# Optimization experiments

Measured on AMD Instinct MI355X. Metric: run time of the kernel, lower is better.

Reference implementation:

```python
import jax, jax.numpy as jnp
import numpy as np

N_NODES = 10000
N_EDGES = 80000
LATENT = 128
OUT_SIZE = 3
NODE_F = 12
EDGE_F = 7
STEPS = 15
LN_EPS = 1e-5


def _mlp(x, W0, b0, W1, b1, W2, b2):
    h = jax.nn.relu(x @ W0 + b0)
    h = jax.nn.relu(h @ W1 + b1)
    return h @ W2 + b2


def _ln(x, g, b):
    m = jnp.mean(x, axis=-1, keepdims=True)
    v = jnp.mean(jnp.square(x - m), axis=-1, keepdims=True)
    return (x - m) * jax.lax.rsqrt(v + LN_EPS) * g + b


def _forward(node_features, edge_features, senders, receivers,
             enW0, enb0, enW1, enb1, enW2, enb2, eng, enbe,
             eeW0, eeb0, eeW1, eeb1, eeW2, eeb2, eeg, eebe,
             beW0, beb0, beW1, beb1, beW2, beb2, beg, bebe,
             bnW0, bnb0, bnW1, bnb1, bnW2, bnb2, bng, bnbe,
             dW0, db0, dW1, db1, dW2, db2):
    # Encoder: node and mesh-edge MLPs with LayerNorm
    nl = _ln(_mlp(node_features, enW0, enb0, enW1, enb1, enW2, enb2), eng, enbe)  # [N, L]
    el = _ln(_mlp(edge_features, eeW0, eeb0, eeW1, eeb1, eeW2, eeb2), eeg, eebe)  # [E, L]

    # Processor: 15 GraphNetBlocks with residual connections, scanned over stacked params
    def block(carry, p):
        n, e = carry
        (eW0, eb0, eW1, eb1, eW2, eb2, eg, ebe,
         nW0, nb0, nW1, nb1, nW2, nb2, ng, nbe) = p
        feat = jnp.concatenate([n[senders], n[receivers], e], axis=-1)  # [E, 3L]
        new_e = _ln(_mlp(feat, eW0, eb0, eW1, eb1, eW2, eb2), eg, ebe)  # [E, L]
        agg = jax.ops.segment_sum(new_e, receivers, num_segments=N_NODES)  # [N, L]
        new_n = _ln(_mlp(jnp.concatenate([n, agg], axis=-1), nW0, nb0, nW1, nb1, nW2, nb2), ng, nbe)
        return (n + new_n, e + new_e), None

    xs = (beW0, beb0, beW1, beb1, beW2, beb2, beg, bebe,
          bnW0, bnb0, bnW1, bnb1, bnW2, bnb2, bng, bnbe)
    (nl, el), _ = jax.lax.scan(jax.checkpoint(block), (nl, el), xs)

    # Decoder: MLP without LayerNorm
    return _mlp(nl, dW0, db0, dW1, db1, dW2, db2)  # [N, OUT_SIZE]


def setup_inputs() -> dict:
    ks = iter(jax.random.split(jax.random.key(0), 32))

    def W(*shape):
        return jax.random.normal(next(ks), shape, jnp.float32) * (1.0 / np.sqrt(shape[-2]))

    z = lambda *s: jnp.zeros(s, jnp.float32)
    o = lambda *s: jnp.ones(s, jnp.float32)
    d = {}
    d['node_features'] = jax.random.normal(next(ks), (N_NODES, NODE_F), jnp.float32)
    d['edge_features'] = jax.random.normal(next(ks), (N_EDGES, EDGE_F), jnp.float32)
    d['senders'] = jax.random.randint(next(ks), (N_EDGES,), 0, N_NODES, jnp.int32)
    d['receivers'] = jax.random.randint(next(ks), (N_EDGES,), 0, N_NODES, jnp.int32)
    d.update(enW0=W(NODE_F, LATENT), enb0=z(LATENT), enW1=W(LATENT, LATENT), enb1=z(LATENT),
             enW2=W(LATENT, LATENT), enb2=z(LATENT), eng=o(LATENT), enbe=z(LATENT))
    d.update(eeW0=W(EDGE_F, LATENT), eeb0=z(LATENT), eeW1=W(LATENT, LATENT), eeb1=z(LATENT),
             eeW2=W(LATENT, LATENT), eeb2=z(LATENT), eeg=o(LATENT), eebe=z(LATENT))
    d.update(beW0=W(STEPS, 3 * LATENT, LATENT), beb0=z(STEPS, LATENT),
             beW1=W(STEPS, LATENT, LATENT), beb1=z(STEPS, LATENT),
             beW2=W(STEPS, LATENT, LATENT), beb2=z(STEPS, LATENT),
             beg=o(STEPS, LATENT), bebe=z(STEPS, LATENT))
    d.update(bnW0=W(STEPS, 2 * LATENT, LATENT), bnb0=z(STEPS, LATENT),
             bnW1=W(STEPS, LATENT, LATENT), bnb1=z(STEPS, LATENT),
             bnW2=W(STEPS, LATENT, LATENT), bnb2=z(STEPS, LATENT),
             bng=o(STEPS, LATENT), bnbe=z(STEPS, LATENT))
    d.update(dW0=W(LATENT, LATENT), db0=z(LATENT), dW1=W(LATENT, LATENT), db1=z(LATENT),
             dW2=W(LATENT, OUT_SIZE), db2=z(OUT_SIZE))
    return d


def reference(node_features, edge_features, senders, receivers,
              enW0, enb0, enW1, enb1, enW2, enb2, eng, enbe,
              eeW0, eeb0, eeW1, eeb1, eeW2, eeb2, eeg, eebe,
              beW0, beb0, beW1, beb1, beW2, beb2, beg, bebe,
              bnW0, bnb0, bnW1, bnb1, bnW2, bnb2, bng, bnbe,
              dW0, db0, dW1, db1, dW2, db2):
    return _forward(node_features, edge_features, senders, receivers,
                    enW0, enb0, enW1, enb1, enW2, enb2, eng, enbe,
                    eeW0, eeb0, eeW1, eeb1, eeW2, eeb2, eeg, eebe,
                    beW0, beb0, beW1, beb1, beW2, beb2, beg, bebe,
                    bnW0, bnb0, bnW1, bnb1, bnW2, bnb2, bng, bnbe,
                    dW0, db0, dW1, db1, dW2, db2)
```

## Files before the change

kernel.cpp:

```cpp
#include <hip/hip_runtime.h>
#include <hip/hip_bf16.h>
#include <stdint.h>

#define N_NODES 10000
#define N_EDGES 80000
#define L 128
#define STEPS 15
#define LN_EPS 1e-5f
#define NTHR 256
#define H_STRIDE 272

typedef short short8 __attribute__((ext_vector_type(8)));
typedef float floatx4 __attribute__((ext_vector_type(4)));

__device__ __forceinline__ float bf2f(const __hip_bfloat16 x) {
    return __bfloat162float(x);
}
__device__ __forceinline__ float ldmix(const void* p, int idx, int isf32) {
    return isf32 ? ((const float*)p)[idx]
                 : bf2f(((const __hip_bfloat16*)p)[idx]);
}

__global__ void detect_dtype(const uint32_t* __restrict__ nf, int* cnt) {
    int c = 0;
    for (int i = blockIdx.x * blockDim.x + threadIdx.x; i < 60000;
         i += gridDim.x * blockDim.x) {
        const uint32_t w = nf[i];
        c += (((w >> 7) & 0xFF) >= 0xC6) + (((w >> 23) & 0xFF) >= 0xC6);
    }
    atomicAdd(cnt, c);
}

#define N_TMATS 14
struct TAll {
    const void* src[N_TMATS];
    long long cum[N_TMATS + 1];
    int K[N_TMATS], N[N_TMATS], Kpad[N_TMATS];
};

__global__ void transpose_all(TAll a, const int* __restrict__ cnt,
                              __hip_bfloat16* __restrict__ pool) {
    const int isf32 = (*cnt > 1000);
    const long long total = a.cum[N_TMATS];
    for (long long i = blockIdx.x * (long long)blockDim.x + threadIdx.x;
         i < total; i += gridDim.x * (long long)blockDim.x) {
        int e = 0;
        #pragma unroll 1
        for (int j = 1; j < N_TMATS; j++) if (i >= a.cum[j]) e = j;
        const long long r = i - a.cum[e];
        const int per = a.N[e] * a.Kpad[e];
        const int m = (int)(r / per);
        const int r2 = (int)(r - (long long)m * per);
        const int nn = r2 / a.Kpad[e];
        const int kk = r2 - nn * a.Kpad[e];
        float v = 0.f;
        if (kk < a.K[e]) v = ldmix(a.src[e], (m * a.K[e] + kk) * a.N[e] + nn, isf32);
        pool[i] = __float2bfloat16(v);
    }
}

__global__ void convert_feats(const void* __restrict__ nf,
                              const void* __restrict__ ef,
                              const int* __restrict__ cnt,
                              const int* __restrict__ elist,
                              __hip_bfloat16* __restrict__ fN,
                              __hip_bfloat16* __restrict__ fE)
{
    const int isf32 = (*cnt > 1000);
    const int totN = N_NODES * 32;
    const int totE = N_EDGES * 32;
    for (int i = blockIdx.x * blockDim.x + threadIdx.x; i < totN + totE;
         i += gridDim.x * blockDim.x) {
        if (i < totN) {
            const int r = i >> 5, c = i & 31;
            fN[i] = __float2bfloat16(c < 12 ? ldmix(nf, r * 12 + c, isf32) : 0.f);
        } else {
            const int j = i - totN;
            const int r = j >> 5, c = j & 31;
            const int e = elist[r];
            fE[j] = __float2bfloat16(c < 7 ? ldmix(ef, e * 7 + c, isf32) : 0.f);
        }
    }
}

__global__ void csr_hist(const int* __restrict__ rcv, int* __restrict__ deg) {
    for (int i = blockIdx.x * blockDim.x + threadIdx.x; i < N_EDGES;
         i += gridDim.x * blockDim.x)
        atomicAdd(&deg[rcv[i]], 1);
}

__global__ void csr_scan(const int* __restrict__ deg, int* __restrict__ rowptr,
                         int* __restrict__ cursor) {
    __shared__ int part[256];
    __shared__ int partx[257];
    const int t = threadIdx.x;
    int s = 0;
    for (int j = 0; j < 40; j++) {
        const int i = t * 40 + j;
        if (i < N_NODES) s += deg[i];
    }
    part[t] = s;
    __syncthreads();
    if (t == 0) {
        int r = 0;
        for (int k = 0; k < 256; k++) { partx[k] = r; r += part[k]; }
        partx[256] = r;
    }
    __syncthreads();
    int run = partx[t];
    for (int j = 0; j < 40; j++) {
        const int i = t * 40 + j;
        if (i < N_NODES) {
            rowptr[i] = run;
            cursor[i] = run;
            run += deg[i];
        }
    }
    if (t == 255) rowptr[N_NODES] = partx[256];
}

__global__ void csr_scatter(const int* __restrict__ rcv, int* __restrict__ cursor,
                            int* __restrict__ elist) {
    for (int i = blockIdx.x * blockDim.x + threadIdx.x; i < N_EDGES;
         i += gridDim.x * blockDim.x) {
        const int p = atomicAdd(&cursor[rcv[i]], 1);
        elist[p] = i;
    }
}

__global__ void sort_meta(const int* __restrict__ snd, const int* __restrict__ rcv,
                          const int* __restrict__ elist,
                          int* __restrict__ ssnd, int* __restrict__ srcv) {
    for (int i = blockIdx.x * blockDim.x + threadIdx.x; i < N_EDGES;
         i += gridDim.x * blockDim.x) {
        const int e = elist[i];
        ssnd[i] = snd[e];
        srcv[i] = rcv[e];
    }
}

__global__ __launch_bounds__(256)
void csr_agg(const int* __restrict__ rowptr,
             const __hip_bfloat16* __restrict__ ln16,
             __hip_bfloat16* __restrict__ agg16)
{
    const int g = threadIdx.x >> 5;
    const int lane = threadIdx.x & 31;
    const int v = blockIdx.x * 8 + g;
    if (v >= N_NODES) return;
    const int c0 = lane * 4;
    float s0 = 0.f, s1 = 0.f, s2 = 0.f, s3 = 0.f;
    int j = rowptr[v];
    const int en = rowptr[v + 1];
    for (; j + 1 < en; j += 2) {
        union { uint2 w; __hip_bfloat16 h[4]; } u0, u1;
        u0.w = *(const uint2*)(ln16 + (size_t)j * L + c0);
        u1.w = *(const uint2*)(ln16 + (size_t)(j + 1) * L + c0);
        s0 += bf2f(u0.h[0]); s1 += bf2f(u0.h[1]); s2 += bf2f(u0.h[2]); s3 += bf2f(u0.h[3]);
        s0 += bf2f(u1.h[0]); s1 += bf2f(u1.h[1]); s2 += bf2f(u1.h[2]); s3 += bf2f(u1.h[3]);
    }
    for (; j < en; j++) {
        union { uint2 w; __hip_bfloat16 h[4]; } u;
        u.w = *(const uint2*)(ln16 + (size_t)j * L + c0);
        s0 += bf2f(u.h[0]); s1 += bf2f(u.h[1]); s2 += bf2f(u.h[2]); s3 += bf2f(u.h[3]);
    }
    union { uint2 w; __hip_bfloat16 h[4]; } o;
    o.h[0] = __float2bfloat16(s0); o.h[1] = __float2bfloat16(s1);
    o.h[2] = __float2bfloat16(s2); o.h[3] = __float2bfloat16(s3);
    *(uint2*)(agg16 + (size_t)v * L + c0) = o.w;
}

enum AMode { A_PLAIN = 0, A_FEAT = 1, A_CAT = 2 };
enum Epi   { E_LN_STORE = 0, E_LN_EDGE = 1, E_LN_NODE = 2, E_DEC = 3 };

template <int AMODE, int EPI, int NL, int RT, int MINW>
__global__ __launch_bounds__(NTHR, MINW)
void fused_mlp(const __hip_bfloat16* __restrict__ A, int lda, int M, int K0,
               const __hip_bfloat16* __restrict__ WT0,
               const __hip_bfloat16* __restrict__ WT1,
               const __hip_bfloat16* __restrict__ WT2,
               const void* __restrict__ b0,
               const void* __restrict__ b1,
               const void* __restrict__ b2,
               const void* __restrict__ g,
               const void* __restrict__ beta,
               int poff,
               const int* __restrict__ cnt,
               const __hip_bfloat16* __restrict__ n16,
               const __hip_bfloat16* __restrict__ e16s,
               const __hip_bfloat16* __restrict__ agg16,
               const int* __restrict__ ssnd,
               const int* __restrict__ srcv,
               float* res32,
               __hip_bfloat16* res16,
               __hip_bfloat16* __restrict__ lnout,
               const void* __restrict__ dW,
               const void* __restrict__ db,
               void* __restrict__ dout)
{
    constexpr int BMv   = 64 * RT;
    constexpr int HW    = RT * 16 * H_STRIDE;
    constexpr int WSOFF = 4 * HW;
    __shared__ __align__(16) char lds[WSOFF + 10240];
    char* AsB = lds;
    char* WsB = lds + WSOFF;

    const int tid  = threadIdx.x;
    const int wv   = tid >> 6;
    const int lane = tid & 63;
    const int quad = lane >> 4;
    const int m15  = lane & 15;
    const int row0 = blockIdx.x * BMv;
    const int isf32 = (*cnt > 1000);

    char* hw = lds + wv * HW;

    const int boff = m15 * 80 + quad * 16;
    int aoff[RT];
    #pragma unroll
    for (int rt = 0; rt < RT; rt++)
        aoff[rt] = (wv * 16 * RT + rt * 16 + m15) * 80 + quad * 16;

    const int aq = tid & 3;
    int arow[RT], sidx[RT], ridx[RT];
    #pragma unroll
    for (int i2 = 0; i2 < RT; i2++) {
        arow[i2] = (i2 * NTHR + tid) >> 2;
        if constexpr (AMODE == A_FEAT) {
            const int rg = row0 + arow[i2];
            sidx[i2] = (rg < M) ? ssnd[rg] : 0;
            ridx[i2] = (rg < M) ? srcv[rg] : 0;
        }
    }

    auto loadA = [&](int k0, int i2) -> int4 {
        const int rg = row0 + arow[i2];
        int4 av = make_int4(0, 0, 0, 0);
        if (rg < M) {
            if constexpr (AMODE == A_PLAIN) {
                av = *(const int4*)(A + (size_t)rg * lda + k0 + aq * 8);
            } else if constexpr (AMODE == A_FEAT) {
                const __hip_bfloat16* sp;
                if (k0 < 2 * L) {
                    const int nd = (k0 < L) ? sidx[i2] : ridx[i2];
                    sp = n16 + (size_t)nd * L + (k0 & (L - 1)) + aq * 8;
                } else {
                    sp = e16s + (size_t)rg * L + (k0 - 2 * L) + aq * 8;
                }
                av = *(const int4*)sp;
            } else {
                const __hip_bfloat16* sp = (k0 < L)
                    ? n16   + (size_t)rg * L + k0 + aq * 8
                    : agg16 + (size_t)rg * L + (k0 - L) + aq * 8;
                av = *(const int4*)sp;
            }
        }
        return av;
    };
    auto loadW = [&](const __hip_bfloat16* WT, int ksz, int k0, int i2) -> int4 {
        const int flat = i2 * NTHR + tid;
        return *(const int4*)(WT + (size_t)(flat >> 2) * ksz + k0 + (flat & 3) * 8);
    };

    floatx4 acc[RT][8];

    #pragma unroll
    for (int rt = 0; rt < RT; rt++)
        #pragma unroll
        for (int ct = 0; ct < 8; ct++) acc[rt][ct] = (floatx4)0.f;

    int4 pA[RT], pW[2];
    #pragma unroll
    for (int i2 = 0; i2 < RT; i2++) pA[i2] = loadA(0, i2);
    pW[0] = loadW(WT0, K0, 0, 0);
    pW[1] = loadW(WT0, K0, 0, 1);

    for (int k0 = 0; k0 < K0; k0 += 32) {
        #pragma unroll
        for (int i2 = 0; i2 < RT; i2++)
            *(int4*)(AsB + arow[i2] * 80 + aq * 16) = pA[i2];
        #pragma unroll
        for (int i2 = 0; i2 < 2; i2++) {
            const int flat = i2 * NTHR + tid;
            *(int4*)(WsB + (flat >> 2) * 80 + (flat & 3) * 16) = pW[i2];
        }
        __syncthreads();
        if (k0 + 32 < K0) {
            #pragma unroll
            for (int i2 = 0; i2 < RT; i2++) pA[i2] = loadA(k0 + 32, i2);
            pW[0] = loadW(WT0, K0, k0 + 32, 0);
            pW[1] = loadW(WT0, K0, k0 + 32, 1);
        }
        short8 a[RT];
        #pragma unroll
        for (int rt = 0; rt < RT; rt++) a[rt] = *(const short8*)(AsB + aoff[rt]);
        #pragma unroll
        for (int ct = 0; ct < 8; ct++) {
            const short8 b = *(const short8*)(WsB + boff + ct * 1280);
            #pragma unroll
            for (int rt = 0; rt < RT; rt++)
                acc[rt][ct] = __builtin_amdgcn_mfma_f32_16x16x32_bf16(a[rt], b, acc[rt][ct], 0, 0, 0);
        }
        __syncthreads();
    }
    {
        float bb[8];
        #pragma unroll
        for (int ct = 0; ct < 8; ct++) bb[ct] = ldmix(b0, poff + ct * 16 + m15, isf32);
        #pragma unroll
        for (int rt = 0; rt < RT; rt++)
            #pragma unroll
            for (int ct = 0; ct < 8; ct++)
                #pragma unroll
                for (int i = 0; i < 4; i++) {
                    const int rl = rt * 16 + quad * 4 + i;
                    const int col = ct * 16 + m15;
                    *(__hip_bfloat16*)(hw + rl * H_STRIDE + col * 2) =
                        __float2bfloat16(fmaxf(acc[rt][ct][i] + bb[ct], 0.f));
                }
    }

    {
        #pragma unroll
        for (int rt = 0; rt < RT; rt++)
            #pragma unroll
            for (int ct = 0; ct < 8; ct++) acc[rt][ct] = (floatx4)0.f;
        short8 af[RT][4];
        #pragma unroll
        for (int rt = 0; rt < RT; rt++)
            #pragma unroll
            for (int c = 0; c < 4; c++)
                af[rt][c] = *(const short8*)(hw + (rt * 16 + m15) * H_STRIDE + c * 64 + quad * 16);
        int4 qW[2];
        qW[0] = loadW(WT1, L, 0, 0);
        qW[1] = loadW(WT1, L, 0, 1);
        for (int c = 0; c < 4; c++) {
            #pragma unroll
            for (int i2 = 0; i2 < 2; i2++) {
                const int flat = i2 * NTHR + tid;
                *(int4*)(WsB + (flat >> 2) * 80 + (flat & 3) * 16) = qW[i2];
            }
            __syncthreads();
            if (c < 3) {
                qW[0] = loadW(WT1, L, (c + 1) * 32, 0);
                qW[1] = loadW(WT1, L, (c + 1) * 32, 1);
            }
            #pragma unroll
            for (int ct = 0; ct < 8; ct++) {
                const short8 b = *(const short8*)(WsB + boff + ct * 1280);
                #pragma unroll
                for (int rt = 0; rt < RT; rt++)
                    acc[rt][ct] = __builtin_amdgcn_mfma_f32_16x16x32_bf16(af[rt][c], b, acc[rt][ct], 0, 0, 0);
            }
            __syncthreads();
        }
        float bb[8];
        #pragma unroll
        for (int ct = 0; ct < 8; ct++) bb[ct] = ldmix(b1, poff + ct * 16 + m15, isf32);
        #pragma unroll
        for (int rt = 0; rt < RT; rt++)
            #pragma unroll
            for (int ct = 0; ct < 8; ct++)
                #pragma unroll
                for (int i = 0; i < 4; i++) {
                    const int rl = rt * 16 + quad * 4 + i;
                    const int col = ct * 16 + m15;
                    *(__hip_bfloat16*)(hw + rl * H_STRIDE + col * 2) =
                        __float2bfloat16(fmaxf(acc[rt][ct][i] + bb[ct], 0.f));
                }
    }

    if constexpr (NL == 3) {
        #pragma unroll
        for (int rt = 0; rt < RT; rt++)
            #pragma unroll
            for (int ct = 0; ct < 8; ct++) acc[rt][ct] = (floatx4)0.f;
        short8 af[RT][4];
        #pragma unroll
        for (int rt = 0; rt < RT; rt++)
            #pragma unroll
            for (int c = 0; c < 4; c++)
                af[rt][c] = *(const short8*)(hw + (rt * 16 + m15) * H_STRIDE + c * 64 + quad * 16);
        int4 qW[2];
        qW[0] = loadW(WT2, L, 0, 0);
        qW[1] = loadW(WT2, L, 0, 1);
        for (int c = 0; c < 4; c++) {
            #pragma unroll
            for (int i2 = 0; i2 < 2; i2++) {
                const int flat = i2 * NTHR + tid;
                *(int4*)(WsB + (flat >> 2) * 80 + (flat & 3) * 16) = qW[i2];
            }
            __syncthreads();
            if (c < 3) {
                qW[0] = loadW(WT2, L, (c + 1) * 32, 0);
                qW[1] = loadW(WT2, L, (c + 1) * 32, 1);
            }
            #pragma unroll
            for (int ct = 0; ct < 8; ct++) {
                const short8 b = *(const short8*)(WsB + boff + ct * 1280);
                #pragma unroll
                for (int rt = 0; rt < RT; rt++)
                    acc[rt][ct] = __builtin_amdgcn_mfma_f32_16x16x32_bf16(af[rt][c], b, acc[rt][ct], 0, 0, 0);
            }
            __syncthreads();
        }
        float bb[8], gg[8], be[8];
        #pragma unroll
        for (int ct = 0; ct < 8; ct++) {
            bb[ct] = ldmix(b2,   poff + ct * 16 + m15, isf32);
            gg[ct] = ldmix(g,    poff + ct * 16 + m15, isf32);
            be[ct] = ldmix(beta, poff + ct * 16 + m15, isf32);
        }
        #pragma unroll
        for (int rt = 0; rt < RT; rt++) {
            #pragma unroll
            for (int i = 0; i < 4; i++) {
                float t[8], s = 0.f, s2 = 0.f;
                #pragma unroll
                for (int ct = 0; ct < 8; ct++) {
                    t[ct] = acc[rt][ct][i] + bb[ct];
                    s  += t[ct];
                    s2 += t[ct] * t[ct];
                }
                #pragma unroll
                for (int m = 1; m < 16; m <<= 1) {
                    s  += __shfl_xor(s,  m, 64);
                    s2 += __shfl_xor(s2, m, 64);
                }
                const float mean = s * (1.f / 128.f);
                const float var  = s2 * (1.f / 128.f) - mean * mean;
                const float inv  = rsqrtf(fmaxf(var, 0.f) + LN_EPS);
                const int rl = wv * 16 * RT + rt * 16 + quad * 4 + i;
                const int rg = row0 + rl;
                if (rg < M) {
                    #pragma unroll
                    for (int ct = 0; ct < 8; ct++) {
                        const int col = ct * 16 + m15;
                        const float o = (t[ct] - mean) * inv * gg[ct] + be[ct];
                        const size_t idx = (size_t)rg * L + col;
                        if constexpr (EPI == E_LN_STORE) {
                            res32[idx] = o;
                            if (res16) res16[idx] = __float2bfloat16(o);
                        } else if constexpr (EPI == E_LN_NODE) {
                            const float nw = res32[idx] + o;
                            res32[idx] = nw;
                            res16[idx] = __float2bfloat16(nw);
                        } else {
                            const float nw = res32[idx] + o;
                            res32[idx] = nw;
                            res16[idx] = __float2bfloat16(nw);
                            lnout[idx] = __float2bfloat16(o);
                        }
                    }
                }
            }
        }
    } else {
        __syncthreads();
        float* Wl = (float*)WsB;
        for (int i = tid; i < 3 * L; i += NTHR) {
            const int o = i / L, k = i - o * L;
            Wl[o * L + k] = ldmix(dW, k * 3 + o, isf32);
        }
        __syncthreads();
        if (tid < BMv) {
            const int rg = row0 + tid;
            if (rg < M) {
                const int wave = tid / (16 * RT);
                const int rw   = tid - wave * 16 * RT;
                const __hip_bfloat16* hr =
                    (const __hip_bfloat16*)(lds + wave * HW + rw * H_STRIDE);
                float s0 = ldmix(db, 0, isf32);
                float s1 = ldmix(db, 1, isf32);
                float s2 = ldmix(db, 2, isf32);
                #pragma unroll 8
                for (int k = 0; k < L; k++) {
                    const float hv = bf2f(hr[k]);
                    s0 += hv * Wl[k];
                    s1 += hv * Wl[L + k];
                    s2 += hv * Wl[2 * L + k];
                }
                if (isf32) {
                    float* o = (float*)dout;
                    o[rg * 3 + 0] = s0; o[rg * 3 + 1] = s1; o[rg * 3 + 2] = s2;
                } else {
                    __hip_bfloat16* o = (__hip_bfloat16*)dout;
                    o[rg * 3 + 0] = __float2bfloat16(s0);
                    o[rg * 3 + 1] = __float2bfloat16(s1);
                    o[rg * 3 + 2] = __float2bfloat16(s2);
                }
            }
        }
    }
}

extern "C" void kernel_launch(void* const* d_in, const int* in_sizes, int n_in,
                              void* d_out, int out_size, void* d_ws, size_t ws_size,
                              hipStream_t stream)
{
    (void)in_sizes; (void)n_in; (void)out_size; (void)ws_size;
    const int* snd = (const int*)d_in[2];
    const int* rcv = (const int*)d_in[3];

    char* ws = (char*)d_ws;
    int* cnt = (int*)ws;                              ws += 256;
    auto takeB = [&](size_t el) {
        __hip_bfloat16* p = (__hip_bfloat16*)ws;
        ws += ((el * 2 + 255) & ~255ull);
        return p;
    };
    auto takeF = [&](size_t el) {
        float* p = (float*)ws;
        ws += ((el * 4 + 255) & ~255ull);
        return p;
    };
    auto takeI = [&](size_t el) {
        int* p = (int*)ws;
        ws += ((el * 4 + 255) & ~255ull);
        return p;
    };

    const int srcIdx[N_TMATS] = {4, 6, 8, 12, 14, 16, 20, 22, 24, 28, 30, 32, 36, 38};
    const int tK[N_TMATS]    = {12, 128, 128, 7, 128, 128, 384, 128, 128, 256, 128, 128, 128, 128};
    const int tKp[N_TMATS]   = {32, 128, 128, 32, 128, 128, 384, 128, 128, 256, 128, 128, 128, 128};
    const int tNm[N_TMATS]   = {1, 1, 1, 1, 1, 1, STEPS, STEPS, STEPS, STEPS, STEPS, STEPS, 1, 1};
    TAll ta;
    long long cum = 0;
    __hip_bfloat16* wmat[N_TMATS];
    __hip_bfloat16* wpool = (__hip_bfloat16*)ws;
    for (int j = 0; j < N_TMATS; j++) {
        ta.src[j] = d_in[srcIdx[j]];
        ta.cum[j] = cum;
        ta.K[j] = tK[j]; ta.N[j] = 128; ta.Kpad[j] = tKp[j];
        wmat[j] = wpool + cum;
        cum += (long long)tNm[j] * 128 * tKp[j];
    }
    ta.cum[N_TMATS] = cum;
    ws += ((cum * 2 + 255) & ~255ull);

    float* n32 = takeF((size_t)N_NODES * L);
    float* e32 = takeF((size_t)N_EDGES * L);
    __hip_bfloat16* n16   = takeB((size_t)N_NODES * L);
    __hip_bfloat16* e16   = takeB((size_t)N_EDGES * L);
    __hip_bfloat16* ln16  = takeB((size_t)N_EDGES * L);
    __hip_bfloat16* agg16 = takeB((size_t)N_NODES * L);
    __hip_bfloat16* fN16  = takeB((size_t)N_NODES * 32);
    __hip_bfloat16* fE16  = takeB((size_t)N_EDGES * 32);
    int* deg    = takeI(N_NODES);
    int* rowptr = takeI(N_NODES + 1);
    int* cursor = takeI(N_NODES);
    int* elist  = takeI(N_EDGES);
    int* ssnd   = takeI(N_EDGES);
    int* srcv   = takeI(N_EDGES);

    const dim3 blk(NTHR);
    const dim3 grdE((N_EDGES + 63) / 64);
    const dim3 grdN((N_NODES + 63) / 64);

    (void)hipMemsetAsync(cnt, 0, sizeof(int), stream);
    (void)hipMemsetAsync(deg, 0, N_NODES * sizeof(int), stream);
    detect_dtype<<<dim3(64), blk, 0, stream>>>((const uint32_t*)d_in[0], cnt);
    transpose_all<<<dim3(512), blk, 0, stream>>>(ta, cnt, wpool);

    csr_hist<<<dim3(80), blk, 0, stream>>>(rcv, deg);
    csr_scan<<<dim3(1), blk, 0, stream>>>(deg, rowptr, cursor);
    csr_scatter<<<dim3(80), blk, 0, stream>>>(rcv, cursor, elist);
    sort_meta<<<dim3(80), blk, 0, stream>>>(snd, rcv, elist, ssnd, srcv);
    convert_feats<<<dim3(256), blk, 0, stream>>>(d_in[0], d_in[1], cnt, elist, fN16, fE16);

    fused_mlp<A_PLAIN, E_LN_STORE, 3, 1, 3><<<grdE, blk, 0, stream>>>(
        fE16, 32, N_EDGES, 32, wmat[3], wmat[4], wmat[5],
        d_in[13], d_in[15], d_in[17], d_in[18], d_in[19], 0, cnt,
        nullptr, nullptr, nullptr, nullptr, nullptr,
        e32, e16, nullptr, nullptr, nullptr, nullptr);
    fused_mlp<A_PLAIN, E_LN_STORE, 3, 1, 3><<<grdN, blk, 0, stream>>>(
        fN16, 32, N_NODES, 32, wmat[0], wmat[1], wmat[2],
        d_in[5], d_in[7], d_in[9], d_in[10], d_in[11], 0, cnt,
        nullptr, nullptr, nullptr, nullptr, nullptr,
        n32, n16, nullptr, nullptr, nullptr, nullptr);

    for (int s = 0; s < STEPS; s++) {
        const int po = s * L;
        fused_mlp<A_FEAT, E_LN_EDGE, 3, 1, 3><<<grdE, blk, 0, stream>>>(
            nullptr, 0, N_EDGES, 384,
            wmat[6] + (size_t)s * 128 * 384,
            wmat[7] + (size_t)s * 128 * 128,
            wmat[8] + (size_t)s * 128 * 128,
            d_in[21], d_in[23], d_in[25], d_in[26], d_in[27], po, cnt,
            n16, e16, nullptr, ssnd, srcv,
            e32, e16, ln16, nullptr, nullptr, nullptr);
        csr_agg<<<dim3((N_NODES + 7) / 8), blk, 0, stream>>>(rowptr, ln16, agg16);
        fused_mlp<A_CAT, E_LN_NODE, 3, 1, 3><<<grdN, blk, 0, stream>>>(
            nullptr, 0, N_NODES, 256,
            wmat[9]  + (size_t)s * 128 * 256,
            wmat[10] + (size_t)s * 128 * 128,
            wmat[11] + (size_t)s * 128 * 128,
            d_in[29], d_in[31], d_in[33], d_in[34], d_in[35], po, cnt,
            n16, nullptr, agg16, nullptr, nullptr,
            n32, n16, nullptr, nullptr, nullptr, nullptr);
    }

    fused_mlp<A_PLAIN, E_DEC, 2, 1, 3><<<grdN, blk, 0, stream>>>(
        n16, L, N_NODES, L, wmat[12], wmat[13], nullptr,
        d_in[37], d_in[39], nullptr, nullptr, nullptr, 0, cnt,
        nullptr, nullptr, nullptr, nullptr, nullptr,
        nullptr, nullptr, nullptr, d_in[40], d_in[41], d_out);
}
```

Before: 1.328 ms.

## Pre-swizzle weights into MFMA fragment order and double-buffer LDS weight tiles

The weight transpose kernel now writes weights in the exact per-lane MFMA B-fragment order, so LDS stores and reads are contiguous 16-byte per-lane accesses. The MLP kernel loads A fragments directly from global memory into registers instead of staging them through LDS. It double-buffers 64-wide K sections of weights in LDS, which roughly halves the barrier count and overlaps the next section's load with the current MFMAs. K0 becomes a template parameter and the RT row-tiling option is removed, at the cost of more LDS per block and scattered direct global gathers for the A operand.

```diff
diff --git a/kernel.cpp b/kernel.cpp
--- a/kernel.cpp
+++ b/kernel.cpp
@@ -50,11 +50,16 @@
         const long long r = i - a.cum[e];
         const int per = a.N[e] * a.Kpad[e];
         const int m = (int)(r / per);
-        const int r2 = (int)(r - (long long)m * per);
-        const int nn = r2 / a.Kpad[e];
-        const int kk = r2 - nn * a.Kpad[e];
+        int r2 = (int)(r - (long long)m * per);
+        const int c2   = r2 >> 12;
+        const int rem  = r2 & 4095;
+        const int ct   = rem >> 9;
+        const int lane = (rem >> 3) & 63;
+        const int j    = rem & 7;
+        const int k    = c2 * 32 + (lane >> 4) * 8 + j;
+        const int col  = ct * 16 + (lane & 15);
         float v = 0.f;
-        if (kk < a.K[e]) v = ldmix(a.src[e], (m * a.K[e] + kk) * a.N[e] + nn, isf32);
+        if (k < a.K[e]) v = ldmix(a.src[e], (m * a.K[e] + k) * a.N[e] + col, isf32);
         pool[i] = __float2bfloat16(v);
     }
 }
@@ -173,9 +178,9 @@
 enum AMode { A_PLAIN = 0, A_FEAT = 1, A_CAT = 2 };
 enum Epi   { E_LN_STORE = 0, E_LN_EDGE = 1, E_LN_NODE = 2, E_DEC = 3 };
 
-template <int AMODE, int EPI, int NL, int RT, int MINW>
-__global__ __launch_bounds__(NTHR, MINW)
-void fused_mlp(const __hip_bfloat16* __restrict__ A, int lda, int M, int K0,
+template <int AMODE, int EPI, int NL, int K0>
+__global__ __launch_bounds__(NTHR, 3)
+void fused_mlp(const __hip_bfloat16* __restrict__ A, int lda, int M,
                const __hip_bfloat16* __restrict__ WT0,
                const __hip_bfloat16* __restrict__ WT1,
                const __hip_bfloat16* __restrict__ WT2,
@@ -198,211 +203,160 @@
                const void* __restrict__ db,
                void* __restrict__ dout)
 {
-    constexpr int BMv   = 64 * RT;
-    constexpr int HW    = RT * 16 * H_STRIDE;
-    constexpr int WSOFF = 4 * HW;
-    __shared__ __align__(16) char lds[WSOFF + 10240];
-    char* AsB = lds;
-    char* WsB = lds + WSOFF;
+    __shared__ __align__(16) char lds[17408 + 32768];
+    char* wbuf = lds + 17408;
 
     const int tid  = threadIdx.x;
     const int wv   = tid >> 6;
     const int lane = tid & 63;
     const int quad = lane >> 4;
     const int m15  = lane & 15;
-    const int row0 = blockIdx.x * BMv;
+    const int row0 = blockIdx.x * 64;
     const int isf32 = (*cnt > 1000);
 
-    char* hw = lds + wv * HW;
-
-    const int boff = m15 * 80 + quad * 16;
-    int aoff[RT];
+    char* hw = lds + wv * 4352;
+
+    const int rw = row0 + wv * 16 + m15;
+    const int rc = rw < M ? rw : M - 1;
+
+    int sI = 0, rI = 0;
+    if constexpr (AMODE == A_FEAT) { sI = ssnd[rc]; rI = srcv[rc]; }
+
+    auto aFrag = [&](int kchunk) -> short8 {
+        const int k0 = kchunk * 32 + quad * 8;
+        const __hip_bfloat16* sp;
+        if constexpr (AMODE == A_PLAIN) {
+            sp = A + (size_t)rc * lda + k0;
+        } else if constexpr (AMODE == A_FEAT) {
+            if (k0 < L)          sp = n16  + (size_t)sI * L + k0;
+            else if (k0 < 2 * L) sp = n16  + (size_t)rI * L + (k0 - L);
+            else                 sp = e16s + (size_t)rc * L + (k0 - 2 * L);
+        } else {
+            if (k0 < L) sp = n16   + (size_t)rc * L + k0;
+            else        sp = agg16 + (size_t)rc * L + (k0 - L);
+        }
+        return *(const short8*)sp;
+    };
+    auto loadW = [&](const __hip_bfloat16* secPtr, int ch, int4* wr) {
+        #pragma unroll
+        for (int it = 0; it < 4; it++)
+            if (it < 2 * ch)
+                wr[it] = *(const int4*)(secPtr + (size_t)wv * ch * 1024 + it * 512 + lane * 8);
+    };
+    auto storeW = [&](int buf, int ch, const int4* wr) {
+        #pragma unroll
+        for (int it = 0; it < 4; it++)
+            if (it < 2 * ch)
+                *(int4*)(wbuf + buf * 16384 + wv * ch * 2048 + it * 1024 + lane * 16) = wr[it];
+    };
+    auto bread = [&](int buf, int kc, int ct) -> short8 {
+        return *(const short8*)(wbuf + buf * 16384 + kc * 8192 + ct * 1024 + lane * 16);
+    };
+
+    constexpr int CH0 = (K0 == 32) ? 1 : 2;
+    constexpr int S0  = (K0 == 32) ? 1 : (K0 / 64);
+
+    int4 wreg[4];
+    short8 aF[2];
+    int buf = 0;
+    floatx4 acc[8];
+
     #pragma unroll
-    for (int rt = 0; rt < RT; rt++)
-        aoff[rt] = (wv * 16 * RT + rt * 16 + m15) * 80 + quad * 16;
-
-    const int aq = tid & 3;
-    int arow[RT], sidx[RT], ridx[RT];
-    #pragma unroll
-    for (int i2 = 0; i2 < RT; i2++) {
-        arow[i2] = (i2 * NTHR + tid) >> 2;
-        if constexpr (AMODE == A_FEAT) {
-            const int rg = row0 + arow[i2];
-            sidx[i2] = (rg < M) ? ssnd[rg] : 0;
-            ridx[i2] = (rg < M) ? srcv[rg] : 0;
-        }
-    }
-
-    auto loadA = [&](int k0, int i2) -> int4 {
-        const int rg = row0 + arow[i2];
-        int4 av = make_int4(0, 0, 0, 0);
-        if (rg < M) {
-            if constexpr (AMODE == A_PLAIN) {
-                av = *(const int4*)(A + (size_t)rg * lda + k0 + aq * 8);
-            } else if constexpr (AMODE == A_FEAT) {
-                const __hip_bfloat16* sp;
-                if (k0 < 2 * L) {
-                    const int nd = (k0 < L) ? sidx[i2] : ridx[i2];
-                    sp = n16 + (size_t)nd * L + (k0 & (L - 1)) + aq * 8;
-                } else {
-                    sp = e16s + (size_t)rg * L + (k0 - 2 * L) + aq * 8;
-                }
-                av = *(const int4*)sp;
-            } else {
-                const __hip_bfloat16* sp = (k0 < L)
-                    ? n16   + (size_t)rg * L + k0 + aq * 8
-                    : agg16 + (size_t)rg * L + (k0 - L) + aq * 8;
-                av = *(const int4*)sp;
-            }
-        }
-        return av;
-    };
-    auto loadW = [&](const __hip_bfloat16* WT, int ksz, int k0, int i2) -> int4 {
-        const int flat = i2 * NTHR + tid;
-        return *(const int4*)(WT + (size_t)(flat >> 2) * ksz + k0 + (flat & 3) * 8);
-    };
-
-    floatx4 acc[RT][8];
-
-    #pragma unroll
-    for (int rt = 0; rt < RT; rt++)
-        #pragma unroll
-        for (int ct = 0; ct < 8; ct++) acc[rt][ct] = (floatx4)0.f;
-
-    int4 pA[RT], pW[2];
-    #pragma unroll
-    for (int i2 = 0; i2 < RT; i2++) pA[i2] = loadA(0, i2);
-    pW[0] = loadW(WT0, K0, 0, 0);
-    pW[1] = loadW(WT0, K0, 0, 1);
-
-    for (int k0 = 0; k0 < K0; k0 += 32) {
-        #pragma unroll
-        for (int i2 = 0; i2 < RT; i2++)
-            *(int4*)(AsB + arow[i2] * 80 + aq * 16) = pA[i2];
-        #pragma unroll
-        for (int i2 = 0; i2 < 2; i2++) {
-            const int flat = i2 * NTHR + tid;
-            *(int4*)(WsB + (flat >> 2) * 80 + (flat & 3) * 16) = pW[i2];
-        }
+    for (int ct = 0; ct < 8; ct++) acc[ct] = (floatx4)0.f;
+
+    loadW(WT0, CH0, wreg);
+    aF[0] = aFrag(0);
+    if constexpr (CH0 == 2) aF[1] = aFrag(1);
+
+    for (int sec = 0; sec < S0; sec++) {
+        storeW(buf, CH0, wreg);
         __syncthreads();
-        if (k0 + 32 < K0) {
-            #pragma unroll
-            for (int i2 = 0; i2 < RT; i2++) pA[i2] = loadA(k0 + 32, i2);
-            pW[0] = loadW(WT0, K0, k0 + 32, 0);
-            pW[1] = loadW(WT0, K0, k0 + 32, 1);
-        }
-        short8 a[RT];
-        #pragma unroll
-        for (int rt = 0; rt < RT; rt++) a[rt] = *(const short8*)(AsB + aoff[rt]);
-        #pragma unroll
-        for (int ct = 0; ct < 8; ct++) {
-            const short8 b = *(const short8*)(WsB + boff + ct * 1280);
-            #pragma unroll
-            for (int rt = 0; rt < RT; rt++)
-                acc[rt][ct] = __builtin_amdgcn_mfma_f32_16x16x32_bf16(a[rt], b, acc[rt][ct], 0, 0, 0);
-        }
-        __syncthreads();
+        const short8 a0 = aF[0];
+        const short8 a1 = aF[1];
+        if (sec + 1 < S0) {
+            loadW(WT0 + (size_t)(sec + 1) * CH0 * 4096, CH0, wreg);
+            aF[0] = aFrag((sec + 1) * CH0);
+            if constexpr (CH0 == 2) aF[1] = aFrag((sec + 1) * CH0 + 1);
+        } else {
+            loadW(WT1, 2, wreg);
+        }
+        #pragma unroll
+        for (int ct = 0; ct < 8; ct++)
+            acc[ct] = __builtin_amdgcn_mfma_f32_16x16x32_bf16(a0, bread(buf, 0, ct), acc[ct], 0, 0, 0);
+        if constexpr (CH0 == 2) {
+            #pragma unroll
+            for (int ct = 0; ct < 8; ct++)
+                acc[ct] = __builtin_amdgcn_mfma_f32_16x16x32_bf16(a1, bread(buf, 1, ct), acc[ct], 0, 0, 0);
+        }
+        buf ^= 1;
     }
     {
         float bb[8];
         #pragma unroll
         for (int ct = 0; ct < 8; ct++) bb[ct] = ldmix(b0, poff + ct * 16 + m15, isf32);
         #pragma unroll
-        for (int rt = 0; rt < RT; rt++)
-            #pragma unroll
-            for (int ct = 0; ct < 8; ct++)
+        for (int ct = 0; ct < 8; ct++)
+            #pragma unroll
+            for (int i = 0; i < 4; i++) {
+                const int rl = quad * 4 + i;
+                const int col = ct * 16 + m15;
+                *(__hip_bfloat16*)(hw + rl * H_STRIDE + col * 2) =
+                    __float2bfloat16(fmaxf(acc[ct][i] + bb[ct], 0.f));
+            }
+    }
+
+    {
+        #pragma unroll
+        for (int ct = 0; ct < 8; ct++) acc[ct] = (floatx4)0.f;
+        short8 af[4];
+        #pragma unroll
+        for (int c = 0; c < 4; c++)
+            af[c] = *(const short8*)(hw + m15 * H_STRIDE + c * 64 + quad * 16);
+        for (int sec = 0; sec < 2; sec++) {
+            storeW(buf, 2, wreg);
+            __syncthreads();
+            if (sec == 0)            loadW(WT1 + 8192, 2, wreg);
+            else if constexpr (NL == 3) loadW(WT2, 2, wreg);
+            #pragma unroll
+            for (int kc = 0; kc < 2; kc++)
                 #pragma unroll
-                for (int i = 0; i < 4; i++) {
-                    const int rl = rt * 16 + quad * 4 + i;
-                    const int col = ct * 16 + m15;
-                    *(__hip_bfloat16*)(hw + rl * H_STRIDE + col * 2) =
-                        __float2bfloat16(fmaxf(acc[rt][ct][i] + bb[ct], 0.f));
-                }
-    }
-
-    {
-        #pragma unroll
-        for (int rt = 0; rt < RT; rt++)
-            #pragma unroll
-            for (int ct = 0; ct < 8; ct++) acc[rt][ct] = (floatx4)0.f;
-        short8 af[RT][4];
-        #pragma unroll
-        for (int rt = 0; rt < RT; rt++)
-            #pragma unroll
-            for (int c = 0; c < 4; c++)
-                af[rt][c] = *(const short8*)(hw + (rt * 16 + m15) * H_STRIDE + c * 64 + quad * 16);
-        int4 qW[2];
-        qW[0] = loadW(WT1, L, 0, 0);
-        qW[1] = loadW(WT1, L, 0, 1);
-        for (int c = 0; c < 4; c++) {
-            #pragma unroll
-            for (int i2 = 0; i2 < 2; i2++) {
-                const int flat = i2 * NTHR + tid;
-                *(int4*)(WsB + (flat >> 2) * 80 + (flat & 3) * 16) = qW[i2];
+                for (int ct = 0; ct < 8; ct++)
+                    acc[ct] = __builtin_amdgcn_mfma_f32_16x16x32_bf16(
+                        af[sec * 2 + kc], bread(buf, kc, ct), acc[ct], 0, 0, 0);
+            buf ^= 1;
+        }
+        float bb[8];
+        #pragma unroll
+        for (int ct = 0; ct < 8; ct++) bb[ct] = ldmix(b1, poff + ct * 16 + m15, isf32);
+        #pragma unroll
+        for (int ct = 0; ct < 8; ct++)
+            #pragma unroll
+            for (int i = 0; i < 4; i++) {
+                const int rl = quad * 4 + i;
+                const int col = ct * 16 + m15;
+                *(__hip_bfloat16*)(hw + rl * H_STRIDE + col * 2) =
+                    __float2bfloat16(fmaxf(acc[ct][i] + bb[ct], 0.f));
             }
+    }
+
+    if constexpr (NL == 3) {
+        #pragma unroll
+        for (int ct = 0; ct < 8; ct++) acc[ct] = (floatx4)0.f;
+        short8 af[4];
+        #pragma unroll
+        for (int c = 0; c < 4; c++)
+            af[c] = *(const short8*)(hw + m15 * H_STRIDE + c * 64 + quad * 16);
+        for (int sec = 0; sec < 2; sec++) {
+            storeW(buf, 2, wreg);
             __syncthreads();
-            if (c < 3) {
-                qW[0] = loadW(WT1, L, (c + 1) * 32, 0);
-                qW[1] = loadW(WT1, L, (c + 1) * 32, 1);
-            }
-            #pragma unroll
-            for (int ct = 0; ct < 8; ct++) {
-                const short8 b = *(const short8*)(WsB + boff + ct * 1280);
+            if (sec == 0) loadW(WT2 + 8192, 2, wreg);
+            #pragma unroll
+            for (int kc = 0; kc < 2; kc++)
                 #pragma unroll
-                for (int rt = 0; rt < RT; rt++)
-                    acc[rt][ct] = __builtin_amdgcn_mfma_f32_16x16x32_bf16(af[rt][c], b, acc[rt][ct], 0, 0, 0);
-            }
-            __syncthreads();
-        }
-        float bb[8];
-        #pragma unroll
-        for (int ct = 0; ct < 8; ct++) bb[ct] = ldmix(b1, poff + ct * 16 + m15, isf32);
-        #pragma unroll
-        for (int rt = 0; rt < RT; rt++)
-            #pragma unroll
-            for (int ct = 0; ct < 8; ct++)
-                #pragma unroll
-                for (int i = 0; i < 4; i++) {
-                    const int rl = rt * 16 + quad * 4 + i;
-                    const int col = ct * 16 + m15;
-                    *(__hip_bfloat16*)(hw + rl * H_STRIDE + col * 2) =
-                        __float2bfloat16(fmaxf(acc[rt][ct][i] + bb[ct], 0.f));
-                }
-    }
-
-    if constexpr (NL == 3) {
-        #pragma unroll
-        for (int rt = 0; rt < RT; rt++)
-            #pragma unroll
-            for (int ct = 0; ct < 8; ct++) acc[rt][ct] = (floatx4)0.f;
-        short8 af[RT][4];
-        #pragma unroll
-        for (int rt = 0; rt < RT; rt++)
-            #pragma unroll
-            for (int c = 0; c < 4; c++)
-                af[rt][c] = *(const short8*)(hw + (rt * 16 + m15) * H_STRIDE + c * 64 + quad * 16);
-        int4 qW[2];
-        qW[0] = loadW(WT2, L, 0, 0);
-        qW[1] = loadW(WT2, L, 0, 1);
-        for (int c = 0; c < 4; c++) {
-            #pragma unroll
-            for (int i2 = 0; i2 < 2; i2++) {
-                const int flat = i2 * NTHR + tid;
-                *(int4*)(WsB + (flat >> 2) * 80 + (flat & 3) * 16) = qW[i2];
-            }
-            __syncthreads();
-            if (c < 3) {
-                qW[0] = loadW(WT2, L, (c + 1) * 32, 0);
-                qW[1] = loadW(WT2, L, (c + 1) * 32, 1);
-            }
-            #pragma unroll
-            for (int ct = 0; ct < 8; ct++) {
-                const short8 b = *(const short8*)(WsB + boff + ct * 1280);
-                #pragma unroll
-                for (int rt = 0; rt < RT; rt++)
-                    acc[rt][ct] = __builtin_amdgcn_mfma_f32_16x16x32_bf16(af[rt][c], b, acc[rt][ct], 0, 0, 0);
-            }
-            __syncthreads();
+                for (int ct = 0; ct < 8; ct++)
+                    acc[ct] = __builtin_amdgcn_mfma_f32_16x16x32_bf16(
+                        af[sec * 2 + kc], bread(buf, kc, ct), acc[ct], 0, 0, 0);
+            buf ^= 1;
         }
         float bb[8], gg[8], be[8];
         #pragma unroll
@@ -412,64 +366,58 @@
             be[ct] = ldmix(beta, poff + ct * 16 + m15, isf32);
         }
         #pragma unroll
-        for (int rt = 0; rt < RT; rt++) {
-            #pragma unroll
-            for (int i = 0; i < 4; i++) {
-                float t[8], s = 0.f, s2 = 0.f;
+        for (int i = 0; i < 4; i++) {
+            float t[8], s = 0.f, s2 = 0.f;
+            #pragma unroll
+            for (int ct = 0; ct < 8; ct++) {
+                t[ct] = acc[ct][i] + bb[ct];
+                s  += t[ct];
+                s2 += t[ct] * t[ct];
+            }
+            #pragma unroll
+            for (int m = 1; m < 16; m <<= 1) {
+                s  += __shfl_xor(s,  m, 64);
+                s2 += __shfl_xor(s2, m, 64);
+            }
+            const float mean = s * (1.f / 128.f);
+            const float var  = s2 * (1.f / 128.f) - mean * mean;
+            const float inv  = rsqrtf(fmaxf(var, 0.f) + LN_EPS);
+            const int rg = row0 + wv * 16 + quad * 4 + i;
+            if (rg < M) {
                 #pragma unroll
                 for (int ct = 0; ct < 8; ct++) {
-                    t[ct] = acc[rt][ct][i] + bb[ct];
-                    s  += t[ct];
-                    s2 += t[ct] * t[ct];
-                }
-                #pragma unroll
-                for (int m = 1; m < 16; m <<= 1) {
-                    s  += __shfl_xor(s,  m, 64);
-                    s2 += __shfl_xor(s2, m, 64);
-                }
-                const float mean = s * (1.f / 128.f);
-                const float var  = s2 * (1.f / 128.f) - mean * mean;
-                const float inv  = rsqrtf(fmaxf(var, 0.f) + LN_EPS);
-                const int rl = wv * 16 * RT + rt * 16 + quad * 4 + i;
-                const int rg = row0 + rl;
-                if (rg < M) {
-                    #pragma unroll
-                    for (int ct = 0; ct < 8; ct++) {
-                        const int col = ct * 16 + m15;
-                        const float o = (t[ct] - mean) * inv * gg[ct] + be[ct];
-                        const size_t idx = (size_t)rg * L + col;
-                        if constexpr (EPI == E_LN_STORE) {
-                            res32[idx] = o;
-                            if (res16) res16[idx] = __float2bfloat16(o);
-                        } else if constexpr (EPI == E_LN_NODE) {
-                            const float nw = res32[idx] + o;
-                            res32[idx] = nw;
-                            res16[idx] = __float2bfloat16(nw);
-                        } else {
-                            const float nw = res32[idx] + o;
-                            res32[idx] = nw;
-                            res16[idx] = __float2bfloat16(nw);
-                            lnout[idx] = __float2bfloat16(o);
-                        }
+                    const int col = ct * 16 + m15;
+                    const float o = (t[ct] - mean) * inv * gg[ct] + be[ct];
+                    const size_t idx = (size_t)rg * L + col;
+                    if constexpr (EPI == E_LN_STORE) {
+                        res32[idx] = o;
+                        if (res16) res16[idx] = __float2bfloat16(o);
+                    } else if constexpr (EPI == E_LN_NODE) {
+                        const float nw = res32[idx] + o;
+                        res32[idx] = nw;
+                        res16[idx] = __float2bfloat16(nw);
+                    } else {
+                        const float nw = res32[idx] + o;
+                        res32[idx] = nw;
+                        res16[idx] = __float2bfloat16(nw);
+                        lnout[idx] = __float2bfloat16(o);
                     }
                 }
             }
         }
     } else {
         __syncthreads();
-        float* Wl = (float*)WsB;
+        float* Wl = (float*)wbuf;
         for (int i = tid; i < 3 * L; i += NTHR) {
             const int o = i / L, k = i - o * L;
             Wl[o * L + k] = ldmix(dW, k * 3 + o, isf32);
         }
         __syncthreads();
-        if (tid < BMv) {
+        if (tid < 64) {
             const int rg = row0 + tid;
             if (rg < M) {
-                const int wave = tid / (16 * RT);
-                const int rw   = tid - wave * 16 * RT;
                 const __hip_bfloat16* hr =
-                    (const __hip_bfloat16*)(lds + wave * HW + rw * H_STRIDE);
+                    (const __hip_bfloat16*)(lds + (tid >> 4) * 4352 + (tid & 15) * H_STRIDE);
                 float s0 = ldmix(db, 0, isf32);
                 float s1 = ldmix(db, 1, isf32);
                 float s2 = ldmix(db, 2, isf32);
@@ -568,21 +516,21 @@
     sort_meta<<<dim3(80), blk, 0, stream>>>(snd, rcv, elist, ssnd, srcv);
     convert_feats<<<dim3(256), blk, 0, stream>>>(d_in[0], d_in[1], cnt, elist, fN16, fE16);
 
-    fused_mlp<A_PLAIN, E_LN_STORE, 3, 1, 3><<<grdE, blk, 0, stream>>>(
-        fE16, 32, N_EDGES, 32, wmat[3], wmat[4], wmat[5],
+    fused_mlp<A_PLAIN, E_LN_STORE, 3, 32><<<grdE, blk, 0, stream>>>(
+        fE16, 32, N_EDGES, wmat[3], wmat[4], wmat[5],
         d_in[13], d_in[15], d_in[17], d_in[18], d_in[19], 0, cnt,
         nullptr, nullptr, nullptr, nullptr, nullptr,
         e32, e16, nullptr, nullptr, nullptr, nullptr);
-    fused_mlp<A_PLAIN, E_LN_STORE, 3, 1, 3><<<grdN, blk, 0, stream>>>(
-        fN16, 32, N_NODES, 32, wmat[0], wmat[1], wmat[2],
+    fused_mlp<A_PLAIN, E_LN_STORE, 3, 32><<<grdN, blk, 0, stream>>>(
+        fN16, 32, N_NODES, wmat[0], wmat[1], wmat[2],
         d_in[5], d_in[7], d_in[9], d_in[10], d_in[11], 0, cnt,
         nullptr, nullptr, nullptr, nullptr, nullptr,
         n32, n16, nullptr, nullptr, nullptr, nullptr);
 
     for (int s = 0; s < STEPS; s++) {
         const int po = s * L;
-        fused_mlp<A_FEAT, E_LN_EDGE, 3, 1, 3><<<grdE, blk, 0, stream>>>(
-            nullptr, 0, N_EDGES, 384,
+        fused_mlp<A_FEAT, E_LN_EDGE, 3, 384><<<grdE, blk, 0, stream>>>(
+            nullptr, 0, N_EDGES,
             wmat[6] + (size_t)s * 128 * 384,
             wmat[7] + (size_t)s * 128 * 128,
             wmat[8] + (size_t)s * 128 * 128,
@@ -590,8 +538,8 @@
             n16, e16, nullptr, ssnd, srcv,
             e32, e16, ln16, nullptr, nullptr, nullptr);
         csr_agg<<<dim3((N_NODES + 7) / 8), blk, 0, stream>>>(rowptr, ln16, agg16);
-        fused_mlp<A_CAT, E_LN_NODE, 3, 1, 3><<<grdN, blk, 0, stream>>>(
-            nullptr, 0, N_NODES, 256,
+        fused_mlp<A_CAT, E_LN_NODE, 3, 256><<<grdN, blk, 0, stream>>>(
+            nullptr, 0, N_NODES,
             wmat[9]  + (size_t)s * 128 * 256,
             wmat[10] + (size_t)s * 128 * 128,
             wmat[11] + (size_t)s * 128 * 128,
@@ -600,8 +548,8 @@
             n32, n16, nullptr, nullptr, nullptr, nullptr);
     }
 
-    fused_mlp<A_PLAIN, E_DEC, 2, 1, 3><<<grdN, blk, 0, stream>>>(
-        n16, L, N_NODES, L, wmat[12], wmat[13], nullptr,
+    fused_mlp<A_PLAIN, E_DEC, 2, 128><<<grdN, blk, 0, stream>>>(
+        n16, 128, N_NODES, wmat[12], wmat[13], nullptr,
         d_in[37], d_in[39], nullptr, nullptr, nullptr, 0, cnt,
         nullptr, nullptr, nullptr, nullptr, nullptr,
         nullptr, nullptr, nullptr, d_in[40], d_in[41], d_out);
```

Result: no change. 1.322 ms (-0.5%).
